# Optimization experiments

Measured on AMD Instinct MI355X. Metric: run time of the kernel, lower is better.

## Reference

```python
import jax, jax.numpy as jnp
import numpy as np

L, D, H, V, TB = 4, 768, 12, 50257, 2048  # n_layer, n_embd, n_head, vocab, block_size


def setup_inputs() -> dict:
    key = jax.random.key(0)
    ks = jax.random.split(key, 12)
    s = 0.02
    def n(k, shape):
        return jax.random.normal(k, shape, jnp.float32) * s
    return dict(
        idx=jax.random.randint(ks[0], (1, 2048), 0, V),
        targets=jax.random.randint(ks[1], (1, 2048), 0, V),
        wte=n(ks[2], (V, D)),
        wpe=n(ks[3], (TB, D)),
        ln1_w=jnp.ones((L, D)), ln1_b=jnp.zeros((L, D)),
        attn_w=n(ks[4], (L, D, 3 * D)), attn_b=jnp.zeros((L, 3 * D)),
        attn_proj_w=n(ks[5], (L, D, D)), attn_proj_b=jnp.zeros((L, D)),
        ln2_w=jnp.ones((L, D)), ln2_b=jnp.zeros((L, D)),
        fc_w=n(ks[6], (L, D, 4 * D)), fc_b=jnp.zeros((L, 4 * D)),
        mlp_proj_w=n(ks[7], (L, 4 * D, D)), mlp_proj_b=jnp.zeros((L, D)),
        lnf_w=jnp.ones((D,)), lnf_b=jnp.zeros((D,)),
        head_w=n(ks[8], (D, V)), head_b=jnp.zeros((V,)),
    )


def _ln(x, w, b, eps=1e-5):
    m = x.mean(-1, keepdims=True)
    v = ((x - m) ** 2).mean(-1, keepdims=True)
    return (x - m) * jax.lax.rsqrt(v + eps) * w + b


def reference(idx, targets, wte, wpe, ln1_w, ln1_b, attn_w, attn_b,
              attn_proj_w, attn_proj_b, ln2_w, ln2_b, fc_w, fc_b,
              mlp_proj_w, mlp_proj_b, lnf_w, lnf_b, head_w, head_b):
    B, T = idx.shape
    Dh = D // H
    x = wte[idx] + wpe[:T]  # [B,T,D]
    mask = jnp.tril(jnp.ones((T, T), bool))
    neg = jnp.finfo(x.dtype).min
    scale = jnp.asarray(1.0 / np.sqrt(Dh), x.dtype)
    for i in range(L):
        h = _ln(x, ln1_w[i], ln1_b[i])
        qkv = h @ attn_w[i] + attn_b[i]
        q, k, v = jnp.split(qkv, 3, axis=-1)
        q = q.reshape(B, T, H, Dh).transpose(0, 2, 1, 3)
        k = k.reshape(B, T, H, Dh).transpose(0, 2, 1, 3)
        v = v.reshape(B, T, H, Dh).transpose(0, 2, 1, 3)
        scores = jnp.einsum('bhqd,bhkd->bhqk', q, k) * scale
        scores = jnp.where(mask, scores, neg)  # causal masked_fill
        attn = jax.nn.softmax(scores, axis=-1)
        o = jnp.einsum('bhqk,bhkd->bhqd', attn, v)
        o = o.transpose(0, 2, 1, 3).reshape(B, T, D)
        x = x + o @ attn_proj_w[i] + attn_proj_b[i]
        h = _ln(x, ln2_w[i], ln2_b[i])
        h = jax.nn.gelu(h @ fc_w[i] + fc_b[i], approximate=True)  # tanh GELU
        x = x + h @ mlp_proj_w[i] + mlp_proj_b[i]
    x = _ln(x, lnf_w, lnf_b)
    logits = x @ head_w + head_b  # [B,T,V]
    logp = jax.nn.log_softmax(logits, axis=-1)
    nll = -jnp.take_along_axis(logp, targets[..., None], axis=-1).squeeze(-1)
    loss = nll.mean()
    return logits, loss
```

## Files before the change

kernel.cpp:

```cpp
#include <hip/hip_runtime.h>
#include <hip/hip_bf16.h>
#include <math.h>

using bf16   = __hip_bfloat16;
using f32x4  = __attribute__((ext_vector_type(4))) float;
using bf16x8 = __attribute__((ext_vector_type(8))) short;
using s16x4  = __attribute__((ext_vector_type(4))) short;

constexpr int SEQ    = 2048;
constexpr int DMODEL = 768;
constexpr int NHEAD  = 12;
constexpr int NV     = 50257;
constexpr int NVPAD  = 50304;
constexpr int NB     = NVPAD / 128;
constexpr int NLAYER = 4;

__device__ __forceinline__ void gload_lds16(const void* g, void* s) {
    __builtin_amdgcn_global_load_lds((const __attribute__((address_space(1))) void*)g,
                                     (__attribute__((address_space(3))) void*)s, 16, 0, 0);
}

__global__ __launch_bounds__(192) void embed_kernel(const int* __restrict__ idx,
                                                    const float* __restrict__ wte,
                                                    const float* __restrict__ wpe,
                                                    float* __restrict__ x) {
    int t = blockIdx.x;
    int tok = idx[t];
    const float4* a = (const float4*)(wte + (size_t)tok * DMODEL);
    const float4* b = (const float4*)(wpe + (size_t)t * DMODEL);
    float4* o = (float4*)(x + (size_t)t * DMODEL);
    int d = threadIdx.x;
    float4 u = a[d], v = b[d];
    u.x += v.x; u.y += v.y; u.z += v.z; u.w += v.w;
    o[d] = u;
}

__global__ __launch_bounds__(256) void ln_kernel(const float* __restrict__ x,
                                                 const float* __restrict__ w,
                                                 const float* __restrict__ b,
                                                 bf16* __restrict__ out) {
    __shared__ float red[8];
    int row = blockIdx.x, tid = threadIdx.x;
    const float* xr = x + (size_t)row * DMODEL;
    float v[3];
    float s = 0.f, ss = 0.f;
#pragma unroll
    for (int j = 0; j < 3; j++) {
        v[j] = xr[tid + j * 256];
        s += v[j];
        ss += v[j] * v[j];
    }
#pragma unroll
    for (int off = 32; off; off >>= 1) {
        s  += __shfl_down(s,  off, 64);
        ss += __shfl_down(ss, off, 64);
    }
    int wid = tid >> 6, lane = tid & 63;
    if (lane == 0) { red[wid] = s; red[4 + wid] = ss; }
    __syncthreads();
    s  = red[0] + red[1] + red[2] + red[3];
    ss = red[4] + red[5] + red[6] + red[7];
    float mean = s * (1.0f / DMODEL);
    float var  = ss * (1.0f / DMODEL) - mean * mean;
    float rstd = rsqrtf(var + 1e-5f);
#pragma unroll
    for (int j = 0; j < 3; j++) {
        int d = tid + j * 256;
        out[(size_t)row * DMODEL + d] = __float2bfloat16((v[j] - mean) * rstd * w[d] + b[d]);
    }
}

__global__ __launch_bounds__(256) void transpb_kernel(const float* __restrict__ W,
                                                      bf16* __restrict__ Wt,
                                                      int K, int N,
                                                      size_t wstride, size_t tstride) {
    __shared__ float t[64][65];
    int l = blockIdx.z;
    W  += (size_t)l * wstride;
    Wt += (size_t)l * tstride;
    int n0 = blockIdx.x << 6, k0 = blockIdx.y << 6;
    int tid = threadIdx.x;
#pragma unroll
    for (int i = 0; i < 16; i++) {
        int id = tid + (i << 8);
        int r = id >> 6, c = id & 63;
        int n = n0 + c;
        t[r][c] = (n < N) ? W[(size_t)(k0 + r) * N + n] : 0.0f;
    }
    __syncthreads();
#pragma unroll
    for (int i = 0; i < 16; i++) {
        int id = tid + (i << 8);
        int nr = id >> 6, kc = id & 63;
        Wt[(size_t)(n0 + nr) * K + k0 + kc] = __float2bfloat16(t[kc][nr]);
    }
}

template <int ACT, int RES, int OBF>
__global__ __launch_bounds__(256) void mgemm_kernel(const short* __restrict__ A,
                                                    const short* __restrict__ Wt,
                                                    const float* __restrict__ bias,
                                                    const float* __restrict__ res,
                                                    float* __restrict__ outf,
                                                    bf16* __restrict__ outb,
                                                    int N, int K) {
    __shared__ short As[2][4096];
    __shared__ short Bs[2][4096];
    int tid = threadIdx.x, lane = tid & 63, wid = tid >> 6;
    int bm = blockIdx.y << 7, bn = blockIdx.x << 7;
    int wr = (wid >> 1) << 6, wc = (wid & 1) << 6;
    f32x4 acc[4][4] = {};
    int rA = tid >> 2, sA = tid & 3;
    int q = lane >> 4, rr = lane & 15;

    auto STAGE = [&](int b, int k0) {
#pragma unroll
        for (int i = 0; i < 2; i++) {
            int r = rA + (i << 6);
            int gc = k0 + ((sA ^ ((r >> 1) & 3)) << 3);
            char* dstA = (char*)As + b * 8192 + (i << 12) + (wid << 10);
            char* dstB = (char*)Bs + b * 8192 + (i << 12) + (wid << 10);
            gload_lds16(A  + (size_t)(bm + r) * K + gc, dstA);
            gload_lds16(Wt + (size_t)(bn + r) * K + gc, dstB);
        }
    };

    STAGE(0, 0);
    int cur = 0;
    for (int k0 = 0; k0 < K; k0 += 32) {
        if (k0 + 32 < K) {
            STAGE(cur ^ 1, k0 + 32);
            asm volatile("s_waitcnt vmcnt(4)" ::: "memory");
        } else {
            asm volatile("s_waitcnt vmcnt(0)" ::: "memory");
        }
        __builtin_amdgcn_s_barrier();
        __builtin_amdgcn_sched_barrier(0);
        bf16x8 af[4], bfr[4];
#pragma unroll
        for (int m = 0; m < 4; m++) {
            int rowa = wr + (m << 4) + rr;
            af[m]  = *(const bf16x8*)((const char*)As + cur * 8192 + rowa * 64 + ((q ^ ((rowa >> 1) & 3)) << 4));
            int rowb = wc + (m << 4) + rr;
            bfr[m] = *(const bf16x8*)((const char*)Bs + cur * 8192 + rowb * 64 + ((q ^ ((rowb >> 1) & 3)) << 4));
        }
#pragma unroll
        for (int m = 0; m < 4; m++)
#pragma unroll
            for (int n = 0; n < 4; n++)
                acc[m][n] = __builtin_amdgcn_mfma_f32_16x16x32_bf16(bfr[n], af[m], acc[m][n], 0, 0, 0);
        __builtin_amdgcn_sched_barrier(0);
        __builtin_amdgcn_s_barrier();
        cur ^= 1;
    }

    int cl = lane & 15, g = lane >> 4;
#pragma unroll
    for (int m = 0; m < 4; m++) {
        int row = bm + wr + (m << 4) + cl;
#pragma unroll
        for (int n = 0; n < 4; n++) {
            int col0 = bn + wc + (n << 4) + (g << 2);
            float4 bv = *(const float4*)&bias[col0];
            f32x4 v = acc[m][n];
            v[0] += bv.x; v[1] += bv.y; v[2] += bv.z; v[3] += bv.w;
            if (RES) {
                float4 rv = *(const float4*)&res[(size_t)row * N + col0];
                v[0] += rv.x; v[1] += rv.y; v[2] += rv.z; v[3] += rv.w;
            }
            if (ACT) {
#pragma unroll
                for (int j = 0; j < 4; j++)
                    v[j] = v[j] / (1.0f + __expf(-1.5957691216057308f * (v[j] + 0.044715f * v[j] * v[j] * v[j])));
            }
            if (OBF) {
                s16x4 pk;
#pragma unroll
                for (int j = 0; j < 4; j++) {
                    bf16 t = __float2bfloat16(v[j]);
                    pk[j] = *reinterpret_cast<short*>(&t);
                }
                *(s16x4*)&outb[(size_t)row * N + col0] = pk;
            } else {
                *(f32x4*)&outf[(size_t)row * N + col0] = v;
            }
        }
    }
}

__global__ __launch_bounds__(256) void head_kernel(const short* __restrict__ A,
                                                   const short* __restrict__ Wt,
                                                   const float* __restrict__ bias,
                                                   float* __restrict__ out,
                                                   float* __restrict__ pm,
                                                   float* __restrict__ ps) {
    __shared__ short As[4096];
    __shared__ short Bs[4096];
    __shared__ float lm[128][2];
    __shared__ float lsum[128][2];
    constexpr int K = DMODEL;
    int bid = blockIdx.x;
    int swz = (bid & 7) * (6288 / 8) + (bid >> 3);
    int bm = (swz & 15) << 7;
    int bxp = swz >> 4;
    int bn = bxp << 7;
    int tid = threadIdx.x, lane = tid & 63, wid = tid >> 6;
    int wr = (wid >> 1) << 6;
    int wc = (wid & 1) << 6;
    f32x4 acc[4][4] = {};
    int rA = tid >> 2, sA = tid & 3;
    int q = lane >> 4, rr = lane & 15;

    for (int k0 = 0; k0 < K; k0 += 32) {
#pragma unroll
        for (int i = 0; i < 2; i++) {
            int r = rA + (i << 6);
            int gc = k0 + ((sA ^ ((r >> 1) & 3)) << 3);
            char* dstA = (char*)As + (i << 12) + (wid << 10);
            char* dstB = (char*)Bs + (i << 12) + (wid << 10);
            gload_lds16(A  + (size_t)(bm + r) * K + gc, dstA);
            gload_lds16(Wt + (size_t)(bn + r) * K + gc, dstB);
        }
        __syncthreads();
        bf16x8 af[4], bfr[4];
#pragma unroll
        for (int m = 0; m < 4; m++) {
            int rowa = wr + (m << 4) + rr;
            af[m]  = *(const bf16x8*)((const char*)As + rowa * 64 + ((q ^ ((rowa >> 1) & 3)) << 4));
            int rowb = wc + (m << 4) + rr;
            bfr[m] = *(const bf16x8*)((const char*)Bs + rowb * 64 + ((q ^ ((rowb >> 1) & 3)) << 4));
        }
#pragma unroll
        for (int m = 0; m < 4; m++)
#pragma unroll
            for (int n = 0; n < 4; n++)
                acc[m][n] = __builtin_amdgcn_mfma_f32_16x16x32_bf16(bfr[n], af[m], acc[m][n], 0, 0, 0);
        __syncthreads();
    }

    int cl = lane & 15, g = lane >> 4;
#pragma unroll
    for (int m = 0; m < 4; m++) {
        int row = bm + wr + (m << 4) + cl;
#pragma unroll
        for (int n = 0; n < 4; n++) {
            int col0 = bn + wc + (n << 4) + (g << 2);
            f32x4 v = acc[m][n];
            if (col0 + 3 < NV) {
                float4 bv = *(const float4*)&bias[col0];
                v[0] += bv.x; v[1] += bv.y; v[2] += bv.z; v[3] += bv.w;
                *(f32x4*)&out[(size_t)row * NV + col0] = v;
            } else {
#pragma unroll
                for (int j = 0; j < 4; j++) {
                    if (col0 + j < NV) {
                        v[j] += bias[col0 + j];
                        out[(size_t)row * NV + col0 + j] = v[j];
                    } else {
                        v[j] = -1e30f;
                    }
                }
            }
            acc[m][n] = v;
        }
    }
#pragma unroll
    for (int m = 0; m < 4; m++) {
        float t = -1e30f;
#pragma unroll
        for (int n = 0; n < 4; n++)
#pragma unroll
            for (int j = 0; j < 4; j++) t = fmaxf(t, acc[m][n][j]);
        t = fmaxf(t, __shfl_xor(t, 16, 64));
        t = fmaxf(t, __shfl_xor(t, 32, 64));
        if (g == 0) lm[wr + (m << 4) + cl][wid & 1] = t;
    }
    __syncthreads();
#pragma unroll
    for (int m = 0; m < 4; m++) {
        int r = wr + (m << 4) + cl;
        float M = fmaxf(lm[r][0], lm[r][1]);
        float s = 0.f;
#pragma unroll
        for (int n = 0; n < 4; n++)
#pragma unroll
            for (int j = 0; j < 4; j++) s += __expf(acc[m][n][j] - M);
        s += __shfl_xor(s, 16, 64);
        s += __shfl_xor(s, 32, 64);
        if (g == 0) lsum[r][wid & 1] = s;
    }
    __syncthreads();
    if (tid < 128) {
        int r = tid;
        pm[(size_t)(bm + r) * NB + bxp] = fmaxf(lm[r][0], lm[r][1]);
        ps[(size_t)(bm + r) * NB + bxp] = lsum[r][0] + lsum[r][1];
    }
}

__global__ __launch_bounds__(256) void lsered_kernel(const float* __restrict__ pm,
                                                     const float* __restrict__ ps,
                                                     float* __restrict__ lse) {
    int row = (blockIdx.x << 2) + (threadIdx.x >> 6);
    int lane = threadIdx.x & 63;
    const float* pmr = pm + (size_t)row * NB;
    const float* psr = ps + (size_t)row * NB;
    float m = -1e30f, s = 0.f;
    for (int j = lane; j < NB; j += 64) {
        float mb = pmr[j], sb = psr[j];
        float M = fmaxf(m, mb);
        s = s * __expf(m - M) + sb * __expf(mb - M);
        m = M;
    }
#pragma unroll
    for (int off = 32; off; off >>= 1) {
        float m2 = __shfl_xor(m, off, 64), s2 = __shfl_xor(s, off, 64);
        float M = fmaxf(m, m2);
        s = s * __expf(m - M) + s2 * __expf(m2 - M);
        m = M;
    }
    if (lane == 0) lse[row] = m + logf(s);
}

__global__ __launch_bounds__(256) void attn_kernel(const short* __restrict__ qkv,
                                                   bf16* __restrict__ o) {
    __shared__ short Ks[8192];
    __shared__ short Vt[8192];
    __shared__ short Ps[8192];
    int qt = gridDim.x - 1 - blockIdx.x;
    int h = blockIdx.y, tid = threadIdx.x;
    int lane = tid & 63, w = tid >> 6;
    int g = lane >> 4, c = lane & 15;
    int q0 = qt << 6;
    int nkt = (qt >> 1) + 1;

    bf16x8 qa[2];
    {
        const short* src = qkv + (size_t)(q0 + w * 16 + c) * 2304 + h * 64 + g * 8;
        qa[0] = *(const bf16x8*)src;
        qa[1] = *(const bf16x8*)(src + 32);
    }
    float l_i[4] = {};
    f32x4 oacc[4] = {};

    for (int kt = 0; kt < nkt; kt++) {
        __syncthreads();
#pragma unroll
        for (int i = 0; i < 4; i++) {
            int r = (tid >> 3) + i * 32;
            int gslot = (tid & 7) ^ ((r & 7) ^ ((r >> 3) & 7));
            gload_lds16(qkv + (size_t)(kt * 128 + r) * 2304 + 768 + h * 64 + gslot * 8,
                        (char*)Ks + tid * 16 + i * 4096);
        }
#pragma unroll
        for (int ci = 0; ci < 4; ci++) {
            int rv = (tid >> 3) + ci * 32;
            bf16x8 vv = *(const bf16x8*)(qkv + (size_t)(kt * 128 + rv) * 2304 + 1536 + h * 64 + (tid & 7) * 8);
            int slot = rv >> 3;
#pragma unroll
            for (int j = 0; j < 8; j++) {
                int row = (tid & 7) * 8 + j;
                int sp = slot ^ ((row & 7) ^ ((row >> 3) & 7));
                Vt[row * 128 + sp * 8 + (rv & 7)] = vv[j];
            }
        }
        __syncthreads();

        f32x4 sacc[8] = {};
#pragma unroll
        for (int n = 0; n < 8; n++) {
#pragma unroll
            for (int ks = 0; ks < 2; ks++) {
                int row = n * 16 + c;
                int sp = (ks * 4 + g) ^ ((row & 7) ^ ((row >> 3) & 7));
                bf16x8 kf = *(const bf16x8*)(Ks + row * 64 + sp * 8);
                sacc[n] = __builtin_amdgcn_mfma_f32_16x16x32_bf16(qa[ks], kf, sacc[n], 0, 0, 0);
            }
        }
#pragma unroll
        for (int n = 0; n < 8; n++)
#pragma unroll
            for (int i = 0; i < 4; i++) {
                float v = sacc[n][i] * 0.125f;
                if (kt == nkt - 1 && (kt * 128 + n * 16 + c > q0 + w * 16 + g * 4 + i)) v = -1e30f;
                sacc[n][i] = v;
            }
#pragma unroll
        for (int i = 0; i < 4; i++) {
            float rs = 0.f;
            int row = g * 4 + i;
            int sw = (row & 7) ^ (row >> 3);
#pragma unroll
            for (int n = 0; n < 8; n++) {
                float p = __expf(sacc[n][i]);
                rs += p;
                int sp = (2 * n + (c >> 3)) ^ sw;
                bf16 pb = __float2bfloat16(p);
                Ps[w * 2048 + row * 128 + sp * 8 + (c & 7)] = *reinterpret_cast<short*>(&pb);
            }
            rs += __shfl_xor(rs, 1, 16);
            rs += __shfl_xor(rs, 2, 16);
            rs += __shfl_xor(rs, 4, 16);
            rs += __shfl_xor(rs, 8, 16);
            l_i[i] += rs;
        }
        bf16x8 pa[4];
#pragma unroll
        for (int ks = 0; ks < 4; ks++) {
            int sw = (c & 7) ^ (c >> 3);
            int sp = (ks * 4 + g) ^ sw;
            pa[ks] = *(const bf16x8*)(Ps + w * 2048 + c * 128 + sp * 8);
        }
#pragma unroll
        for (int n = 0; n < 4; n++) {
#pragma unroll
            for (int ks = 0; ks < 4; ks++) {
                int row = n * 16 + c;
                int sp = (ks * 4 + g) ^ ((row & 7) ^ ((row >> 3) & 7));
                bf16x8 vf = *(const bf16x8*)(Vt + row * 128 + sp * 8);
                oacc[n] = __builtin_amdgcn_mfma_f32_16x16x32_bf16(pa[ks], vf, oacc[n], 0, 0, 0);
            }
        }
    }
#pragma unroll
    for (int i = 0; i < 4; i++) {
        float inv = 1.0f / l_i[i];
#pragma unroll
        for (int n = 0; n < 4; n++)
            o[(size_t)(q0 + w * 16 + g * 4 + i) * DMODEL + h * 64 + n * 16 + c] =
                __float2bfloat16(oacc[n][i] * inv);
    }
}

__global__ __launch_bounds__(256) void loss_kernel(const float* __restrict__ logits,
                                                   const float* __restrict__ lse,
                                                   const int* __restrict__ targets,
                                                   float* __restrict__ out) {
    __shared__ float red[4];
    int tid = threadIdx.x;
    float acc = 0.f;
    for (int t = tid; t < SEQ; t += 256)
        acc += lse[t] - logits[(size_t)t * NV + targets[t]];
#pragma unroll
    for (int off = 32; off; off >>= 1) acc += __shfl_down(acc, off, 64);
    int wid = tid >> 6, lane = tid & 63;
    if (lane == 0) red[wid] = acc;
    __syncthreads();
    if (tid == 0) out[0] = (red[0] + red[1] + red[2] + red[3]) * (1.0f / SEQ);
}

extern "C" void kernel_launch(void* const* d_in, const int* in_sizes, int n_in,
                              void* d_out, int out_size, void* d_ws, size_t ws_size,
                              hipStream_t stream) {
    const int*   idx         = (const int*)d_in[0];
    const int*   targets     = (const int*)d_in[1];
    const float* wte         = (const float*)d_in[2];
    const float* wpe         = (const float*)d_in[3];
    const float* ln1_w       = (const float*)d_in[4];
    const float* ln1_b       = (const float*)d_in[5];
    const float* attn_w      = (const float*)d_in[6];
    const float* attn_b      = (const float*)d_in[7];
    const float* attn_proj_w = (const float*)d_in[8];
    const float* attn_proj_b = (const float*)d_in[9];
    const float* ln2_w       = (const float*)d_in[10];
    const float* ln2_b       = (const float*)d_in[11];
    const float* fc_w        = (const float*)d_in[12];
    const float* fc_b        = (const float*)d_in[13];
    const float* mlp_proj_w  = (const float*)d_in[14];
    const float* mlp_proj_b  = (const float*)d_in[15];
    const float* lnf_w       = (const float*)d_in[16];
    const float* lnf_b       = (const float*)d_in[17];
    const float* head_w      = (const float*)d_in[18];
    const float* head_b      = (const float*)d_in[19];

    float* logits = (float*)d_out;
    float* loss   = logits + (size_t)SEQ * NV;

    char* p = (char*)d_ws;
    float* x    = (float*)p;  p += (size_t)SEQ * DMODEL * 4;
    bf16*  h    = (bf16*)p;   p += (size_t)SEQ * DMODEL * 2;
    bf16*  o    = (bf16*)p;   p += (size_t)SEQ * DMODEL * 2;
    bf16*  qkvb = (bf16*)p;   p += (size_t)SEQ * 2304 * 2;
    bf16*  fcb  = (bf16*)p;   p += (size_t)SEQ * 3072 * 2;
    float* lse  = (float*)p;  p += (size_t)SEQ * 4;
    float* pm   = (float*)p;  p += (size_t)SEQ * NB * 4;
    float* ps   = (float*)p;  p += (size_t)SEQ * NB * 4;
    bf16*  Wt   = (bf16*)p;

    bf16* wtA = Wt;
    bf16* wtP = wtA + (size_t)4 * 2304 * 768;
    bf16* wtF = wtP + (size_t)4 * 768 * 768;
    bf16* wtM = wtF + (size_t)4 * 3072 * 768;

    embed_kernel<<<SEQ, 192, 0, stream>>>(idx, wte, wpe, x);

    transpb_kernel<<<dim3(2304 / 64, DMODEL / 64, 4), 256, 0, stream>>>(
        attn_w, wtA, DMODEL, 2304, (size_t)DMODEL * 2304, (size_t)2304 * DMODEL);
    transpb_kernel<<<dim3(DMODEL / 64, DMODEL / 64, 4), 256, 0, stream>>>(
        attn_proj_w, wtP, DMODEL, DMODEL, (size_t)DMODEL * DMODEL, (size_t)DMODEL * DMODEL);
    transpb_kernel<<<dim3(3072 / 64, DMODEL / 64, 4), 256, 0, stream>>>(
        fc_w, wtF, DMODEL, 3072, (size_t)DMODEL * 3072, (size_t)3072 * DMODEL);
    transpb_kernel<<<dim3(DMODEL / 64, 3072 / 64, 4), 256, 0, stream>>>(
        mlp_proj_w, wtM, 3072, DMODEL, (size_t)3072 * DMODEL, (size_t)DMODEL * 3072);

    for (int l = 0; l < NLAYER; l++) {
        ln_kernel<<<SEQ, 256, 0, stream>>>(x, ln1_w + l * DMODEL, ln1_b + l * DMODEL, h);
        mgemm_kernel<0, 0, 1><<<dim3(2304 / 128, SEQ / 128), 256, 0, stream>>>(
            (const short*)h, (const short*)(wtA + (size_t)l * 2304 * DMODEL),
            attn_b + l * 2304, nullptr, nullptr, qkvb, 2304, DMODEL);
        attn_kernel<<<dim3(SEQ / 64, NHEAD), 256, 0, stream>>>((const short*)qkvb, o);
        mgemm_kernel<0, 1, 0><<<dim3(DMODEL / 128, SEQ / 128), 256, 0, stream>>>(
            (const short*)o, (const short*)(wtP + (size_t)l * DMODEL * DMODEL),
            attn_proj_b + l * DMODEL, x, x, nullptr, DMODEL, DMODEL);
        ln_kernel<<<SEQ, 256, 0, stream>>>(x, ln2_w + l * DMODEL, ln2_b + l * DMODEL, h);
        mgemm_kernel<1, 0, 1><<<dim3(3072 / 128, SEQ / 128), 256, 0, stream>>>(
            (const short*)h, (const short*)(wtF + (size_t)l * 3072 * DMODEL),
            fc_b + l * 3072, nullptr, nullptr, fcb, 3072, DMODEL);
        mgemm_kernel<0, 1, 0><<<dim3(DMODEL / 128, SEQ / 128), 256, 0, stream>>>(
            (const short*)fcb, (const short*)(wtM + (size_t)l * DMODEL * 3072),
            mlp_proj_b + l * DMODEL, x, x, nullptr, DMODEL, 3072);
    }

    ln_kernel<<<SEQ, 256, 0, stream>>>(x, lnf_w, lnf_b, h);
    transpb_kernel<<<dim3(NVPAD / 64, DMODEL / 64, 1), 256, 0, stream>>>(
        head_w, Wt, DMODEL, NV, 0, 0);
    head_kernel<<<dim3(NB * 16), 256, 0, stream>>>(
        (const short*)h, (const short*)Wt, head_b, logits, pm, ps);
    lsered_kernel<<<SEQ / 4, 256, 0, stream>>>(pm, ps, lse);
    loss_kernel<<<1, 256, 0, stream>>>(logits, lse, targets, loss);
}
```

Measured before the change: 1.240 ms.

## Split-K the residual projection GEMMs with a separate reduction kernel

The attention-output and MLP down-projection GEMMs (N=768) launch only 96 tiles, too few to fill the GPU. They now run as a 3-way split-K kernel that writes fp32 partials to scratch, followed by a row-wise kernel that adds the bias, the partials and the residual into x. This triples the block count, at the cost of extra partial-sum memory traffic and one more launch per GEMM.

```diff
diff --git a/kernel.cpp b/kernel.cpp
--- a/kernel.cpp
+++ b/kernel.cpp
@@ -14,6 +14,7 @@
 constexpr int NVPAD  = 50304;
 constexpr int NB     = NVPAD / 128;
 constexpr int NLAYER = 4;
+constexpr int KSPLIT = 3;
 
 __device__ __forceinline__ void gload_lds16(const void* g, void* s) {
     __builtin_amdgcn_global_load_lds((const __attribute__((address_space(1))) void*)g,
@@ -186,6 +187,92 @@
             }
         }
     }
+}
+
+__global__ __launch_bounds__(256) void mgemmp_kernel(const short* __restrict__ A,
+                                                     const short* __restrict__ Wt,
+                                                     float* __restrict__ partial,
+                                                     int N, int Kc, int Kstride) {
+    __shared__ short As[2][4096];
+    __shared__ short Bs[2][4096];
+    int tid = threadIdx.x, lane = tid & 63, wid = tid >> 6;
+    int bm = blockIdx.y << 7, bn = blockIdx.x << 7;
+    int z = blockIdx.z;
+    const short* Ab  = A  + (size_t)z * Kc;
+    const short* Wb  = Wt + (size_t)z * Kc;
+    int wr = (wid >> 1) << 6, wc = (wid & 1) << 6;
+    f32x4 acc[4][4] = {};
+    int rA = tid >> 2, sA = tid & 3;
+    int q = lane >> 4, rr = lane & 15;
+
+    auto STAGE = [&](int b, int k0) {
+#pragma unroll
+        for (int i = 0; i < 2; i++) {
+            int r = rA + (i << 6);
+            int gc = k0 + ((sA ^ ((r >> 1) & 3)) << 3);
+            char* dstA = (char*)As + b * 8192 + (i << 12) + (wid << 10);
+            char* dstB = (char*)Bs + b * 8192 + (i << 12) + (wid << 10);
+            gload_lds16(Ab + (size_t)(bm + r) * Kstride + gc, dstA);
+            gload_lds16(Wb + (size_t)(bn + r) * Kstride + gc, dstB);
+        }
+    };
+
+    STAGE(0, 0);
+    int cur = 0;
+    for (int k0 = 0; k0 < Kc; k0 += 32) {
+        if (k0 + 32 < Kc) {
+            STAGE(cur ^ 1, k0 + 32);
+            asm volatile("s_waitcnt vmcnt(4)" ::: "memory");
+        } else {
+            asm volatile("s_waitcnt vmcnt(0)" ::: "memory");
+        }
+        __builtin_amdgcn_s_barrier();
+        __builtin_amdgcn_sched_barrier(0);
+        bf16x8 af[4], bfr[4];
+#pragma unroll
+        for (int m = 0; m < 4; m++) {
+            int rowa = wr + (m << 4) + rr;
+            af[m]  = *(const bf16x8*)((const char*)As + cur * 8192 + rowa * 64 + ((q ^ ((rowa >> 1) & 3)) << 4));
+            int rowb = wc + (m << 4) + rr;
+            bfr[m] = *(const bf16x8*)((const char*)Bs + cur * 8192 + rowb * 64 + ((q ^ ((rowb >> 1) & 3)) << 4));
+        }
+#pragma unroll
+        for (int m = 0; m < 4; m++)
+#pragma unroll
+            for (int n = 0; n < 4; n++)
+                acc[m][n] = __builtin_amdgcn_mfma_f32_16x16x32_bf16(bfr[n], af[m], acc[m][n], 0, 0, 0);
+        __builtin_amdgcn_sched_barrier(0);
+        __builtin_amdgcn_s_barrier();
+        cur ^= 1;
+    }
+
+    float* outz = partial + (size_t)z * SEQ * DMODEL;
+    int cl = lane & 15, g = lane >> 4;
+#pragma unroll
+    for (int m = 0; m < 4; m++) {
+        int row = bm + wr + (m << 4) + cl;
+#pragma unroll
+        for (int n = 0; n < 4; n++) {
+            int col0 = bn + wc + (n << 4) + (g << 2);
+            *(f32x4*)&outz[(size_t)row * N + col0] = acc[m][n];
+        }
+    }
+}
+
+__global__ __launch_bounds__(192) void kred_kernel(const float* __restrict__ partial,
+                                                   const float* __restrict__ bias,
+                                                   float* __restrict__ x) {
+    int row = blockIdx.x, t = threadIdx.x;
+    size_t off = (size_t)row * DMODEL + t * 4;
+    f32x4 v = *(f32x4*)&x[off];
+    float4 b = *(const float4*)&bias[t * 4];
+    v[0] += b.x; v[1] += b.y; v[2] += b.z; v[3] += b.w;
+#pragma unroll
+    for (int z = 0; z < KSPLIT; z++) {
+        f32x4 p = *(const f32x4*)&partial[(size_t)z * SEQ * DMODEL + off];
+        v[0] += p[0]; v[1] += p[1]; v[2] += p[2]; v[3] += p[3];
+    }
+    *(f32x4*)&x[off] = v;
 }
 
 __global__ __launch_bounds__(256) void head_kernel(const short* __restrict__ A,
@@ -490,6 +577,7 @@
     bf16* wtP = wtA + (size_t)4 * 2304 * 768;
     bf16* wtF = wtP + (size_t)4 * 768 * 768;
     bf16* wtM = wtF + (size_t)4 * 3072 * 768;
+    float* kscr = (float*)(wtM + (size_t)4 * 768 * 3072);
 
     embed_kernel<<<SEQ, 192, 0, stream>>>(idx, wte, wpe, x);
 
@@ -508,16 +596,18 @@
             (const short*)h, (const short*)(wtA + (size_t)l * 2304 * DMODEL),
             attn_b + l * 2304, nullptr, nullptr, qkvb, 2304, DMODEL);
         attn_kernel<<<dim3(SEQ / 64, NHEAD), 256, 0, stream>>>((const short*)qkvb, o);
-        mgemm_kernel<0, 1, 0><<<dim3(DMODEL / 128, SEQ / 128), 256, 0, stream>>>(
+        mgemmp_kernel<<<dim3(DMODEL / 128, SEQ / 128, KSPLIT), 256, 0, stream>>>(
             (const short*)o, (const short*)(wtP + (size_t)l * DMODEL * DMODEL),
-            attn_proj_b + l * DMODEL, x, x, nullptr, DMODEL, DMODEL);
+            kscr, DMODEL, DMODEL / KSPLIT, DMODEL);
+        kred_kernel<<<SEQ, 192, 0, stream>>>(kscr, attn_proj_b + l * DMODEL, x);
         ln_kernel<<<SEQ, 256, 0, stream>>>(x, ln2_w + l * DMODEL, ln2_b + l * DMODEL, h);
         mgemm_kernel<1, 0, 1><<<dim3(3072 / 128, SEQ / 128), 256, 0, stream>>>(
             (const short*)h, (const short*)(wtF + (size_t)l * 3072 * DMODEL),
             fc_b + l * 3072, nullptr, nullptr, fcb, 3072, DMODEL);
-        mgemm_kernel<0, 1, 0><<<dim3(DMODEL / 128, SEQ / 128), 256, 0, stream>>>(
+        mgemmp_kernel<<<dim3(DMODEL / 128, SEQ / 128, KSPLIT), 256, 0, stream>>>(
             (const short*)fcb, (const short*)(wtM + (size_t)l * DMODEL * 3072),
-            mlp_proj_b + l * DMODEL, x, x, nullptr, DMODEL, 3072);
+            kscr, DMODEL, 3072 / KSPLIT, 3072);
+        kred_kernel<<<SEQ, 192, 0, stream>>>(kscr, mlp_proj_b + l * DMODEL, x);
     }
 
     ln_kernel<<<SEQ, 256, 0, stream>>>(x, lnf_w, lnf_b, h);
```

Result: faster. 1.121 ms (-9.6%).
